# Optimization experiments

Measured on AMD Instinct MI355X. Metric: run time of the kernel, lower is better.

The kernel has to match this reference:

```python
import math
import jax, jax.numpy as jnp
import numpy as np

HIDDEN = 2880
HEAD_DIM = 64
N_HEADS = 64
N_KV = 8
Q_MULT = N_HEADS // N_KV  # 8
QKV_DIM = HEAD_DIM * (N_HEADS + 2 * N_KV)  # 5120
SLIDING_WINDOW = 128
SM_SCALE = 1.0 / math.sqrt(HEAD_DIM)
ROPE_BASE = 150000.0
ROPE_SCALING = 32.0
INIT_CTX = 4096
NTK_ALPHA = 1.0
NTK_BETA = 32.0
EPS = 1e-5
N_TOKENS = 1536


def rope_tables(n):
    # YaRN-style inv_freq mixing (scaling_factor > 1 branch)
    d = HEAD_DIM
    freq = ROPE_BASE ** (jnp.arange(0, d, 2, dtype=jnp.float32) / d)
    concentration = 0.1 * math.log(ROPE_SCALING) + 1.0
    d_half = d / 2
    low = d_half * math.log(INIT_CTX / (NTK_BETA * 2 * math.pi)) / math.log(ROPE_BASE)
    high = d_half * math.log(INIT_CTX / (NTK_ALPHA * 2 * math.pi)) / math.log(ROPE_BASE)
    interpolation = 1.0 / (ROPE_SCALING * freq)
    extrapolation = 1.0 / freq
    ramp = (jnp.arange(d_half, dtype=jnp.float32) - low) / (high - low)
    mask = 1.0 - jnp.clip(ramp, 0.0, 1.0)
    inv_freq = interpolation * (1.0 - mask) + extrapolation * mask
    t = jnp.arange(n, dtype=jnp.float32)
    freqs = t[:, None] * inv_freq[None, :]  # (n, d/2)
    return jnp.cos(freqs) * concentration, jnp.sin(freqs) * concentration


def apply_rotary(x, cos, sin):
    # x: (n, H, d); cos/sin: (n, d/2)
    c = cos[:, None, :]
    s = sin[:, None, :]
    x1, x2 = jnp.split(x, 2, axis=-1)
    return jnp.concatenate([x1 * c - x2 * s, x2 * c + x1 * s], axis=-1)


def setup_inputs() -> dict:
    key = jax.random.key(0)
    ks = jax.random.split(key, 7)
    x = jax.random.normal(ks[0], (N_TOKENS, HIDDEN), dtype=jnp.float32)
    norm_scale = jnp.ones((HIDDEN,), dtype=jnp.float32)
    qkv_w = jax.random.normal(ks[1], (QKV_DIM, HIDDEN), dtype=jnp.float32) * 0.02
    qkv_b = jax.random.normal(ks[2], (QKV_DIM,), dtype=jnp.float32) * 0.02
    out_w = jax.random.normal(ks[3], (HIDDEN, HEAD_DIM * N_HEADS), dtype=jnp.float32) * 0.02
    out_b = jax.random.normal(ks[4], (HIDDEN,), dtype=jnp.float32) * 0.02
    sinks = jax.random.normal(ks[5], (N_HEADS,), dtype=jnp.float32)
    return {"x": x, "norm_scale": norm_scale, "qkv_w": qkv_w, "qkv_b": qkv_b,
            "out_w": out_w, "out_b": out_b, "sinks": sinks}


def reference(x, norm_scale, qkv_w, qkv_b, out_w, out_b, sinks):
    n = x.shape[0]
    # RMSNorm (fp32)
    t = x * jax.lax.rsqrt(jnp.mean(x * x, axis=-1, keepdims=True) + EPS) * norm_scale
    # fused QKV projection
    qkv = t @ qkv_w.T + qkv_b  # (n, QKV_DIM)
    q = qkv[:, : N_HEADS * HEAD_DIM].reshape(n, N_KV, Q_MULT, HEAD_DIM)
    k = qkv[:, N_HEADS * HEAD_DIM : (N_HEADS + N_KV) * HEAD_DIM].reshape(n, N_KV, HEAD_DIM)
    v = qkv[:, (N_HEADS + N_KV) * HEAD_DIM :].reshape(n, N_KV, HEAD_DIM)
    # RoPE
    cos, sin = rope_tables(n)
    q = apply_rotary(q.reshape(n, N_HEADS, HEAD_DIM), cos, sin).reshape(n, N_KV, Q_MULT, HEAD_DIM)
    k = apply_rotary(k, cos, sin)
    # attention with causal + sliding-window mask and sink logits
    i = jnp.arange(n)[:, None]
    j = jnp.arange(n)[None, :]
    allowed = (j <= i) & (j > i - SLIDING_WINDOW)
    mask = jnp.where(allowed, 0.0, -jnp.inf).astype(jnp.float32)  # (q, k)
    scores = jnp.einsum('qhmd,khd->hmqk', q, k) * SM_SCALE + mask[None, None, :, :]
    s = sinks.reshape(N_KV, Q_MULT, 1, 1)
    s = jnp.broadcast_to(s, (N_KV, Q_MULT, n, 1))
    logits = jnp.concatenate([scores, s], axis=-1)
    w = jax.nn.softmax(logits, axis=-1)[..., :-1]  # drop sink column
    attn = jnp.einsum('hmqk,khd->qhmd', w, v).reshape(n, N_HEADS * HEAD_DIM)
    # output projection + residual
    return x + attn @ out_w.T + out_b
```

## Files before the change

### kernel.cpp

```cpp
#include <hip/hip_runtime.h>

typedef __attribute__((ext_vector_type(8))) short bf16x8;
typedef __attribute__((ext_vector_type(4))) float f32x4;

#define HIDDEN 2880
#define QKV_DIM 5120
#define NH 64
#define NKV 8
#define HD 64
#define ATT_DIM 4096
#define WINDOW 128
#define SM_SCALE 0.125f

__device__ __forceinline__ ushort f2bf(float f) {
  union { float f; unsigned u; } a; a.f = f;
  unsigned r = a.u + 0x7fffu + ((a.u >> 16) & 1u);
  return (ushort)(r >> 16);
}
__device__ __forceinline__ float bf2f(ushort u) {
  union { unsigned u; float f; } a; a.u = ((unsigned)u) << 16;
  return a.f;
}

__device__ __forceinline__ void gload_lds16(const void* g, void* l) {
  __builtin_amdgcn_global_load_lds((const __attribute__((address_space(1))) void*)g,
                                   (__attribute__((address_space(3))) void*)l, 16, 0, 0);
}

__global__ __launch_bounds__(256)
void norm_cvt(const float* __restrict__ x, const float* __restrict__ scale,
              ushort* __restrict__ t, int n,
              const float* __restrict__ w, ushort* __restrict__ wout, int n4w) {
  int tid = threadIdx.x;
  if ((int)blockIdx.x >= n) {
    int i = ((int)blockIdx.x - n) * 256 + tid;
    int stride = (gridDim.x - n) * 256;
    for (; i < n4w; i += stride) {
      float4 v = ((const float4*)w)[i];
      ushort4 o = { f2bf(v.x), f2bf(v.y), f2bf(v.z), f2bf(v.w) };
      ((ushort4*)wout)[i] = o;
    }
    return;
  }
  int row = blockIdx.x;
  const float4* xr = (const float4*)(x + (size_t)row * HIDDEN);
  float4 a0 = xr[tid];
  float4 a1 = xr[tid + 256];
  bool has2 = tid < 208;
  float4 a2 = has2 ? xr[tid + 512] : float4{0.f, 0.f, 0.f, 0.f};
  float ss = a0.x*a0.x + a0.y*a0.y + a0.z*a0.z + a0.w*a0.w
           + a1.x*a1.x + a1.y*a1.y + a1.z*a1.z + a1.w*a1.w
           + a2.x*a2.x + a2.y*a2.y + a2.z*a2.z + a2.w*a2.w;
  for (int m = 1; m < 64; m <<= 1) ss += __shfl_xor(ss, m, 64);
  __shared__ float red[4];
  if ((tid & 63) == 0) red[tid >> 6] = ss;
  __syncthreads();
  ss = red[0] + red[1] + red[2] + red[3];
  float r = rsqrtf(ss / (float)HIDDEN + 1e-5f);
  ushort4* tr = (ushort4*)(t + (size_t)row * HIDDEN);
  const float4* sc4 = (const float4*)scale;
  {
    float4 s = sc4[tid];
    ushort4 o = { f2bf(a0.x*r*s.x), f2bf(a0.y*r*s.y), f2bf(a0.z*r*s.z), f2bf(a0.w*r*s.w) };
    tr[tid] = o;
  }
  {
    float4 s = sc4[tid + 256];
    ushort4 o = { f2bf(a1.x*r*s.x), f2bf(a1.y*r*s.y), f2bf(a1.z*r*s.z), f2bf(a1.w*r*s.w) };
    tr[tid + 256] = o;
  }
  if (has2) {
    float4 s = sc4[tid + 512];
    ushort4 o = { f2bf(a2.x*r*s.x), f2bf(a2.y*r*s.y), f2bf(a2.z*r*s.z), f2bf(a2.w*r*s.w) };
    tr[tid + 512] = o;
  }
}

template <int MASK_N>
__global__ __launch_bounds__(512)
void gemm_8p(const ushort* __restrict__ A, const ushort* __restrict__ B,
             ushort* __restrict__ P, int M, int N, int K, int NSK) {
  __shared__ __align__(16) ushort Al[2][256 * 64];
  __shared__ __align__(16) ushort Bl[2][256 * 64];
  const int tid = threadIdx.x;
  const int wave = tid >> 6, lane = tid & 63;
  const int l15 = lane & 15, hi = lane >> 4;

  int nwg = gridDim.x, orig = blockIdx.x;
  int q8 = nwg >> 3, r8 = nwg & 7, xcd = orig & 7, seq = orig >> 3;
  int swz = (xcd < r8 ? xcd * (q8 + 1) : r8 * (q8 + 1) + (xcd - r8) * q8) + seq;
  int nm = M >> 8;
  int bm = swz % nm, bn = swz / nm;
  const int row0 = bm * 256, col0 = bn * 256;
  const int sk = blockIdx.y;
  const int NTtot = K >> 6;
  const int tt0 = sk * NTtot / NSK, tt1 = (sk + 1) * NTtot / NSK;
  ushort* Pp = P + (size_t)sk * M * N;

  const int wrow = (wave >> 2) * 128;
  const int wcol = (wave & 3) * 64;
  const int srow = lane >> 3;
  const int schunk = (lane & 7) ^ srow;

  f32x4 acc[8][4] = {};

  auto stageA = [&](int t, int r) {
    int row = row0 + r * 64 + wave * 8 + srow;
    gload_lds16(A + (size_t)row * K + (t << 6) + schunk * 8,
                &Al[t & 1][(r * 64 + wave * 8) * 64]);
  };
  auto stageB = [&](int t, int r) {
    int brow = col0 + r * 64 + wave * 8 + srow;
    if (MASK_N) { if (brow > N - 1) brow = N - 1; }
    gload_lds16(B + (size_t)brow * K + (t << 6) + schunk * 8,
                &Bl[t & 1][(r * 64 + wave * 8) * 64]);
  };
  auto stageAll = [&](int t) {
#pragma unroll
    for (int r = 0; r < 4; ++r) { stageA(t, r); stageB(t, r); }
  };
  auto LDA = [&](bf16x8 (&dst)[4][2], int mh, const char* base) {
#pragma unroll
    for (int mt = 0; mt < 4; ++mt)
#pragma unroll
      for (int ks = 0; ks < 2; ++ks) {
        int rr = wrow + mh * 64 + mt * 16 + l15;
        int off = (rr * 128 + ks * 64 + hi * 16) ^ ((rr & 7) << 4);
        dst[mt][ks] = *(const bf16x8*)(base + off);
      }
  };
  auto LDB = [&](bf16x8 (&dst)[2][2], int nh, const char* base) {
#pragma unroll
    for (int nt = 0; nt < 2; ++nt)
#pragma unroll
      for (int ks = 0; ks < 2; ++ks) {
        int rr = wcol + nh * 32 + nt * 16 + l15;
        int off = (rr * 128 + ks * 64 + hi * 16) ^ ((rr & 7) << 4);
        dst[nt][ks] = *(const bf16x8*)(base + off);
      }
  };
  auto MMA = [&](bf16x8 (&a)[4][2], bf16x8 (&b)[2][2], int mh, int nh) {
    __builtin_amdgcn_s_setprio(1);
#pragma unroll
    for (int ks = 0; ks < 2; ++ks)
#pragma unroll
      for (int nt = 0; nt < 2; ++nt)
#pragma unroll
        for (int mt = 0; mt < 4; ++mt)
          acc[mh * 4 + mt][nh * 2 + nt] = __builtin_amdgcn_mfma_f32_16x16x32_bf16(
              a[mt][ks], b[nt][ks], acc[mh * 4 + mt][nh * 2 + nt], 0, 0, 0);
    __builtin_amdgcn_s_setprio(0);
  };

  stageAll(tt0);
  bool two = (tt1 - tt0 > 1);
  if (two) {
    stageAll(tt0 + 1);
    asm volatile("s_waitcnt vmcnt(8)" ::: "memory");
  } else {
    asm volatile("s_waitcnt vmcnt(0)" ::: "memory");
  }
  __builtin_amdgcn_s_barrier();

  for (int t = tt0; t < tt1; ++t) {
    const char* Ab = (const char*)&Al[t & 1][0];
    const char* Bb = (const char*)&Bl[t & 1][0];
    bool pre = (t + 2 < tt1);
    bf16x8 afr[4][2], bf0[2][2], bf1[2][2];
    LDA(afr, 0, Ab);
    LDB(bf0, 0, Bb);
    __builtin_amdgcn_s_barrier();
    MMA(afr, bf0, 0, 0);
    __builtin_amdgcn_s_barrier();
    LDB(bf1, 1, Bb);
    if (pre) { stageA(t + 2, 0); stageA(t + 2, 2); }
    __builtin_amdgcn_s_barrier();
    MMA(afr, bf1, 0, 1);
    __builtin_amdgcn_s_barrier();
    LDA(afr, 1, Ab);
    if (pre) { stageB(t + 2, 0); stageB(t + 2, 1); stageB(t + 2, 2); stageB(t + 2, 3); }
    __builtin_amdgcn_s_barrier();
    MMA(afr, bf1, 1, 1);
    __builtin_amdgcn_s_barrier();
    if (pre) { stageA(t + 2, 1); stageA(t + 2, 3); }
    __builtin_amdgcn_s_barrier();
    MMA(afr, bf0, 1, 0);
    if (pre) asm volatile("s_waitcnt vmcnt(8)" ::: "memory");
    else     asm volatile("s_waitcnt vmcnt(0)" ::: "memory");
    __builtin_amdgcn_s_barrier();
  }

#pragma unroll
  for (int mtg = 0; mtg < 8; ++mtg) {
#pragma unroll
    for (int nt = 0; nt < 4; ++nt) {
#pragma unroll
      for (int rr = 0; rr < 4; ++rr) {
        int row = row0 + wrow + mtg * 16 + (hi << 2) + rr;
        int col = col0 + wcol + nt * 16 + l15;
        if (!MASK_N || col < N) Pp[(size_t)row * N + col] = f2bf(acc[mtg][nt][rr]);
      }
    }
  }
}

__global__ __launch_bounds__(256)
void reduce_out(const float* __restrict__ x, const float* __restrict__ b,
                const ushort* __restrict__ p, int nsk, size_t stride,
                float* __restrict__ out, int n4, int N) {
  int i = blockIdx.x * blockDim.x + threadIdx.x;
  if (i >= n4) return;
  float4 v = ((const float4*)x)[i];
  int col = (i * 4) % N;
  float4 bb = *(const float4*)(b + col);
  v.x += bb.x; v.y += bb.y; v.z += bb.z; v.w += bb.w;
  for (int s = 0; s < nsk; ++s) {
    ushort4 pv = *(const ushort4*)(p + s * stride + (size_t)i * 4);
    v.x += bf2f(pv.x); v.y += bf2f(pv.y); v.z += bf2f(pv.z); v.w += bf2f(pv.w);
  }
  ((float4*)out)[i] = v;
}

__global__ __launch_bounds__(256)
void rope_split(const ushort* __restrict__ p, size_t stride, const float* __restrict__ qkvb,
                ushort* __restrict__ qb, ushort* __restrict__ kb, ushort* __restrict__ vb) {
  int tok = blockIdx.x;
  int tid = threadIdx.x;
  __shared__ float cs[32], sn[32];
  if (tid < 32) {
    float d = (float)tid;
    float freq = powf(150000.0f, d / 32.0f);
    float conc = 0.1f * logf(32.0f) + 1.0f;
    float lg = logf(150000.0f);
    float low = 32.0f * logf(4096.0f / (32.0f * 6.2831853f)) / lg;
    float high = 32.0f * logf(4096.0f / 6.2831853f) / lg;
    float ramp = (d - low) / (high - low);
    float cl = fminf(fmaxf(ramp, 0.0f), 1.0f);
    float mask = 1.0f - cl;
    float inv_freq = (1.0f - mask) / (32.0f * freq) + mask / freq;
    float fr = (float)tok * inv_freq;
    cs[tid] = cosf(fr) * conc;
    sn[tid] = sinf(fr) * conc;
  }
  __syncthreads();
  const ushort* r0 = p + (size_t)tok * QKV_DIM;
  const ushort* r1 = r0 + stride;
  auto ld = [&](int c) { return bf2f(r0[c]) + bf2f(r1[c]) + qkvb[c]; };
#pragma unroll
  for (int it = 0; it < 8; ++it) {
    int pp = tid + it * 256;
    int hd = pp >> 5, d = pp & 31;
    float x1 = ld(hd * 64 + d), x2 = ld(hd * 64 + d + 32);
    float c = cs[d], s = sn[d];
    size_t o = ((size_t)tok * NH + hd) * HD + d;
    qb[o] = f2bf(x1 * c - x2 * s);
    qb[o + 32] = f2bf(x2 * c + x1 * s);
  }
  {
    int pp = tid;
    int hd = pp >> 5, d = pp & 31;
    float x1 = ld(4096 + hd * 64 + d), x2 = ld(4096 + hd * 64 + d + 32);
    float c = cs[d], s = sn[d];
    size_t o = ((size_t)tok * NKV + hd) * HD + d;
    kb[o] = f2bf(x1 * c - x2 * s);
    kb[o + 32] = f2bf(x2 * c + x1 * s);
  }
#pragma unroll
  for (int it = 0; it < 2; ++it) {
    int pp = tid + it * 256;
    vb[(size_t)tok * (NKV * HD) + pp] = f2bf(ld(4608 + pp));
  }
}

__global__ __launch_bounds__(512)
void attn_cvt(const ushort* __restrict__ qb, const ushort* __restrict__ kb,
              const ushort* __restrict__ vb, const float* __restrict__ sinks,
              ushort* __restrict__ attn, int n, int nattn,
              const float* __restrict__ w, ushort* __restrict__ wout, int n4w) {
  __shared__ __align__(16) ushort Kl[160 * 64];
  __shared__ __align__(16) ushort Vt[64 * 168];
  __shared__ __align__(16) ushort Pl[8][16 * 40];
  int tid = threadIdx.x;
  if ((int)blockIdx.x >= nattn) {
    int i = ((int)blockIdx.x - nattn) * 512 + tid;
    int stride = (gridDim.x - nattn) * 512;
    for (; i < n4w; i += stride) {
      float4 v = ((const float4*)w)[i];
      ushort4 o = { f2bf(v.x), f2bf(v.y), f2bf(v.z), f2bf(v.w) };
      ((ushort4*)wout)[i] = o;
    }
    return;
  }
  int wave = tid >> 6, lane = tid & 63;
  int l15 = lane & 15, hi = lane >> 4;
  int qstart = ((int)blockIdx.x >> 3) * 16;
  int kv = (int)blockIdx.x & 7;
  int head = kv * 8 + wave;
  int key0 = qstart - 128;

  for (int i = 0; i < 3; ++i) {
    int rowb = i * 64 + wave * 8;
    if (rowb < 160) {
      int r = rowb + (lane >> 3);
      int gj = key0 + r; if (gj < 0) gj = 0;
      int chunk = (lane & 7) ^ (lane >> 3);
      gload_lds16(kb + ((size_t)gj * NKV + kv) * HD + chunk * 8, Kl + rowb * 64);
    }
  }
  for (int e = tid; e < 160 * 16; e += 512) {
    int j = e >> 4, d4 = (e & 15) << 2;
    int gj = key0 + j; if (gj < 0) gj = 0;
    ushort4 v = *(const ushort4*)(vb + ((size_t)gj * NKV + kv) * HD + d4);
    Vt[(d4 + 0) * 168 + j] = v.x;
    Vt[(d4 + 1) * 168 + j] = v.y;
    Vt[(d4 + 2) * 168 + j] = v.z;
    Vt[(d4 + 3) * 168 + j] = v.w;
  }
  bf16x8 qf[2];
#pragma unroll
  for (int ks = 0; ks < 2; ++ks) {
    int r = qstart + l15;
    int kk = ks * 32 + hi * 8;
    qf[ks] = *(const bf16x8*)(qb + ((size_t)r * NH + head) * HD + kk);
  }
  __syncthreads();

  f32x4 s[10] = {};
#pragma unroll
  for (int nt = 0; nt < 10; ++nt) {
#pragma unroll
    for (int ks = 0; ks < 2; ++ks) {
      int r = nt * 16 + l15;
      int off = (r * 128 + (ks * 32 + hi * 8) * 2) ^ ((r & 7) << 4);
      bf16x8 kf = *(const bf16x8*)((const char*)Kl + off);
      s[nt] = __builtin_amdgcn_mfma_f32_16x16x32_bf16(qf[ks], kf, s[nt], 0, 0, 0);
    }
  }

  float lrow[4];
  float snk = sinks[head];
#pragma unroll
  for (int r = 0; r < 4; ++r) {
    int i = qstart + hi * 4 + r;
    float mx = -1e30f;
#pragma unroll
    for (int nt = 0; nt < 10; ++nt) {
      int j = key0 + nt * 16 + l15;
      bool ok = (j >= 0) && (j <= i) && (j > i - WINDOW);
      float val = ok ? s[nt][r] * SM_SCALE : -1e30f;
      s[nt][r] = val;
      mx = fmaxf(mx, val);
    }
    mx = fmaxf(mx, __shfl_xor(mx, 1, 64));
    mx = fmaxf(mx, __shfl_xor(mx, 2, 64));
    mx = fmaxf(mx, __shfl_xor(mx, 4, 64));
    mx = fmaxf(mx, __shfl_xor(mx, 8, 64));
    mx = fmaxf(mx, snk);
    float sum = 0.f;
#pragma unroll
    for (int nt = 0; nt < 10; ++nt) {
      float pv = __expf(s[nt][r] - mx);
      s[nt][r] = pv;
      sum += pv;
    }
    sum += __shfl_xor(sum, 1, 64);
    sum += __shfl_xor(sum, 2, 64);
    sum += __shfl_xor(sum, 4, 64);
    sum += __shfl_xor(sum, 8, 64);
    sum += __expf(snk - mx);
    lrow[r] = sum;
  }

  f32x4 o[4] = {};
#pragma unroll
  for (int kc = 0; kc < 5; ++kc) {
#pragma unroll
    for (int t2 = 0; t2 < 2; ++t2) {
      int nt = kc * 2 + t2;
#pragma unroll
      for (int r = 0; r < 4; ++r)
        Pl[wave][(hi * 4 + r) * 40 + t2 * 16 + l15] = f2bf(s[nt][r]);
    }
    bf16x8 pa = *(const bf16x8*)(&Pl[wave][l15 * 40 + hi * 8]);
#pragma unroll
    for (int nt = 0; nt < 4; ++nt) {
      int d = nt * 16 + l15;
      int kk = kc * 32 + hi * 8;
      bf16x8 vf = *(const bf16x8*)(&Vt[d * 168 + kk]);
      o[nt] = __builtin_amdgcn_mfma_f32_16x16x32_bf16(pa, vf, o[nt], 0, 0, 0);
    }
  }

#pragma unroll
  for (int nt = 0; nt < 4; ++nt)
#pragma unroll
    for (int r = 0; r < 4; ++r) {
      int row = qstart + hi * 4 + r;
      int d = nt * 16 + l15;
      float val = o[nt][r] / lrow[r];
      attn[((size_t)row * NH + head) * HD + d] = f2bf(val);
    }
}

extern "C" void kernel_launch(void* const* d_in, const int* in_sizes, int n_in,
                              void* d_out, int out_size, void* d_ws, size_t ws_size,
                              hipStream_t stream) {
  const float* x      = (const float*)d_in[0];
  const float* nscale = (const float*)d_in[1];
  const float* qkv_w  = (const float*)d_in[2];
  const float* qkv_b  = (const float*)d_in[3];
  const float* out_w  = (const float*)d_in[4];
  const float* out_b  = (const float*)d_in[5];
  const float* sinks  = (const float*)d_in[6];
  float* out = (float*)d_out;
  int n = in_sizes[0] / HIDDEN;

  char* ws = (char*)d_ws;
  size_t off = 0;
  auto alloc = [&](size_t bytes) {
    char* p = ws + off;
    off += (bytes + 255) & ~(size_t)255;
    return p;
  };
  ushort* t_bf    = (ushort*)alloc((size_t)n * HIDDEN * 2);
  ushort* qkvw_bf = (ushort*)alloc((size_t)QKV_DIM * HIDDEN * 2);
  ushort* outw_bf = (ushort*)alloc((size_t)HIDDEN * ATT_DIM * 2);
  ushort* q_bf    = (ushort*)alloc((size_t)n * NH * HD * 2);
  ushort* k_bf    = (ushort*)alloc((size_t)n * NKV * HD * 2);
  ushort* v_bf    = (ushort*)alloc((size_t)n * NKV * HD * 2);
  ushort* attn    = (ushort*)alloc((size_t)n * ATT_DIM * 2);
  size_t qkv_ps = (size_t)n * QKV_DIM;
  size_t out_ps = (size_t)n * HIDDEN;
  size_t pelems = 2 * qkv_ps > 3 * out_ps ? 2 * qkv_ps : 3 * out_ps;
  ushort* partials = (ushort*)alloc(pelems * 2);

  norm_cvt<<<n + 1024, 256, 0, stream>>>(x, nscale, t_bf, n,
                                         qkv_w, qkvw_bf, QKV_DIM * HIDDEN / 4);
  gemm_8p<0><<<dim3((n / 256) * (QKV_DIM / 256), 2), 512, 0, stream>>>(
      t_bf, qkvw_bf, partials, n, QKV_DIM, HIDDEN, 2);
  rope_split<<<n, 256, 0, stream>>>(partials, qkv_ps, qkv_b, q_bf, k_bf, v_bf);
  int nattn = (n / 16) * NKV;
  attn_cvt<<<nattn + 320, 512, 0, stream>>>(q_bf, k_bf, v_bf, sinks, attn, n, nattn,
                                            out_w, outw_bf, HIDDEN * ATT_DIM / 4);
  gemm_8p<1><<<dim3((n / 256) * 12, 3), 512, 0, stream>>>(
      attn, outw_bf, partials, n, HIDDEN, ATT_DIM, 3);
  reduce_out<<<(n * HIDDEN / 4 + 255) / 256, 256, 0, stream>>>(
      x, out_b, partials, 3, out_ps, out, n * HIDDEN / 4, HIDDEN);
}
```

Baseline: 171.1 us.

## Fuse split-K reduction, bias and RoPE into the attention kernel

```diff
diff --git a/kernel.cpp b/kernel.cpp
--- a/kernel.cpp
+++ b/kernel.cpp
@@ -221,107 +221,119 @@
   ((float4*)out)[i] = v;
 }
 
-__global__ __launch_bounds__(256)
-void rope_split(const ushort* __restrict__ p, size_t stride, const float* __restrict__ qkvb,
-                ushort* __restrict__ qb, ushort* __restrict__ kb, ushort* __restrict__ vb) {
-  int tok = blockIdx.x;
+__global__ __launch_bounds__(512)
+void attn_cvt(const ushort* __restrict__ p, size_t stride, const float* __restrict__ qkvb,
+              const float* __restrict__ sinks, ushort* __restrict__ attn, int n, int nattn,
+              const float* __restrict__ w, ushort* __restrict__ wout, int n4w) {
+  __shared__ __align__(16) ushort Kl[160 * 64];
+  __shared__ __align__(16) ushort Vt[64 * 168];
+  __shared__ __align__(16) ushort Pl[8][16 * 40];
+  __shared__ float invf[32];
+  __shared__ float conc_s;
   int tid = threadIdx.x;
-  __shared__ float cs[32], sn[32];
+  if ((int)blockIdx.x >= nattn) {
+    int i = ((int)blockIdx.x - nattn) * 512 + tid;
+    int gstride = (gridDim.x - nattn) * 512;
+    for (; i < n4w; i += gstride) {
+      float4 v = ((const float4*)w)[i];
+      ushort4 o = { f2bf(v.x), f2bf(v.y), f2bf(v.z), f2bf(v.w) };
+      ((ushort4*)wout)[i] = o;
+    }
+    return;
+  }
+  int wave = tid >> 6, lane = tid & 63;
+  int l15 = lane & 15, hi = lane >> 4;
+  int qstart = ((int)blockIdx.x >> 3) * 16;
+  int kv = (int)blockIdx.x & 7;
+  int head = kv * 8 + wave;
+  int key0 = qstart - 128;
+
   if (tid < 32) {
     float d = (float)tid;
     float freq = powf(150000.0f, d / 32.0f);
-    float conc = 0.1f * logf(32.0f) + 1.0f;
     float lg = logf(150000.0f);
     float low = 32.0f * logf(4096.0f / (32.0f * 6.2831853f)) / lg;
     float high = 32.0f * logf(4096.0f / 6.2831853f) / lg;
     float ramp = (d - low) / (high - low);
     float cl = fminf(fmaxf(ramp, 0.0f), 1.0f);
     float mask = 1.0f - cl;
-    float inv_freq = (1.0f - mask) / (32.0f * freq) + mask / freq;
-    float fr = (float)tok * inv_freq;
-    cs[tid] = cosf(fr) * conc;
-    sn[tid] = sinf(fr) * conc;
+    invf[tid] = (1.0f - mask) / (32.0f * freq) + mask / freq;
+    if (tid == 0) conc_s = 0.1f * logf(32.0f) + 1.0f;
   }
   __syncthreads();
-  const ushort* r0 = p + (size_t)tok * QKV_DIM;
-  const ushort* r1 = r0 + stride;
-  auto ld = [&](int c) { return bf2f(r0[c]) + bf2f(r1[c]) + qkvb[c]; };
-#pragma unroll
-  for (int it = 0; it < 8; ++it) {
-    int pp = tid + it * 256;
-    int hd = pp >> 5, d = pp & 31;
-    float x1 = ld(hd * 64 + d), x2 = ld(hd * 64 + d + 32);
-    float c = cs[d], s = sn[d];
-    size_t o = ((size_t)tok * NH + hd) * HD + d;
-    qb[o] = f2bf(x1 * c - x2 * s);
-    qb[o + 32] = f2bf(x2 * c + x1 * s);
-  }
-  {
-    int pp = tid;
-    int hd = pp >> 5, d = pp & 31;
-    float x1 = ld(4096 + hd * 64 + d), x2 = ld(4096 + hd * 64 + d + 32);
-    float c = cs[d], s = sn[d];
-    size_t o = ((size_t)tok * NKV + hd) * HD + d;
-    kb[o] = f2bf(x1 * c - x2 * s);
-    kb[o + 32] = f2bf(x2 * c + x1 * s);
-  }
-#pragma unroll
-  for (int it = 0; it < 2; ++it) {
-    int pp = tid + it * 256;
-    vb[(size_t)tok * (NKV * HD) + pp] = f2bf(ld(4608 + pp));
-  }
-}
-
-__global__ __launch_bounds__(512)
-void attn_cvt(const ushort* __restrict__ qb, const ushort* __restrict__ kb,
-              const ushort* __restrict__ vb, const float* __restrict__ sinks,
-              ushort* __restrict__ attn, int n, int nattn,
-              const float* __restrict__ w, ushort* __restrict__ wout, int n4w) {
-  __shared__ __align__(16) ushort Kl[160 * 64];
-  __shared__ __align__(16) ushort Vt[64 * 168];
-  __shared__ __align__(16) ushort Pl[8][16 * 40];
-  int tid = threadIdx.x;
-  if ((int)blockIdx.x >= nattn) {
-    int i = ((int)blockIdx.x - nattn) * 512 + tid;
-    int stride = (gridDim.x - nattn) * 512;
-    for (; i < n4w; i += stride) {
-      float4 v = ((const float4*)w)[i];
-      ushort4 o = { f2bf(v.x), f2bf(v.y), f2bf(v.z), f2bf(v.w) };
-      ((ushort4*)wout)[i] = o;
-    }
-    return;
-  }
-  int wave = tid >> 6, lane = tid & 63;
-  int l15 = lane & 15, hi = lane >> 4;
-  int qstart = ((int)blockIdx.x >> 3) * 16;
-  int kv = (int)blockIdx.x & 7;
-  int head = kv * 8 + wave;
-  int key0 = qstart - 128;
+  float conc = conc_s;
+
+  const ushort* r0b = p;
+  const ushort* r1b = p + stride;
 
   for (int i = 0; i < 3; ++i) {
-    int rowb = i * 64 + wave * 8;
-    if (rowb < 160) {
-      int r = rowb + (lane >> 3);
-      int gj = key0 + r; if (gj < 0) gj = 0;
-      int chunk = (lane & 7) ^ (lane >> 3);
-      gload_lds16(kb + ((size_t)gj * NKV + kv) * HD + chunk * 8, Kl + rowb * 64);
+    int task = tid + i * 512;
+    if (task < 1280) {
+      int rb = task >> 3, ch = task & 7;
+      int gj = key0 + rb; if (gj < 0) gj = 0;
+      size_t base = (size_t)gj * QKV_DIM + 4096 + kv * 64;
+      int d0 = ch * 8, d0p = d0 ^ 32;
+      bf16x8 a0 = *(const bf16x8*)(r0b + base + d0);
+      bf16x8 a1 = *(const bf16x8*)(r1b + base + d0);
+      bf16x8 b0 = *(const bf16x8*)(r0b + base + d0p);
+      bf16x8 b1 = *(const bf16x8*)(r1b + base + d0p);
+      bf16x8 o;
+#pragma unroll
+      for (int j = 0; j < 8; ++j) {
+        float xv = bf2f((ushort)a0[j]) + bf2f((ushort)a1[j]) + qkvb[4096 + kv * 64 + d0 + j];
+        float yv = bf2f((ushort)b0[j]) + bf2f((ushort)b1[j]) + qkvb[4096 + kv * 64 + d0p + j];
+        int d31 = (d0 + j) & 31;
+        float fr = (float)gj * invf[d31];
+        float c, s;
+        __sincosf(fr, &s, &c);
+        c *= conc; s *= conc;
+        float v = (d0 < 32) ? (xv * c - yv * s) : (xv * c + yv * s);
+        o[j] = (short)f2bf(v);
+      }
+      int off = (rb * 128 + ch * 16) ^ ((rb & 7) << 4);
+      *(bf16x8*)((char*)Kl + off) = o;
     }
   }
   for (int e = tid; e < 160 * 16; e += 512) {
     int j = e >> 4, d4 = (e & 15) << 2;
     int gj = key0 + j; if (gj < 0) gj = 0;
-    ushort4 v = *(const ushort4*)(vb + ((size_t)gj * NKV + kv) * HD + d4);
-    Vt[(d4 + 0) * 168 + j] = v.x;
-    Vt[(d4 + 1) * 168 + j] = v.y;
-    Vt[(d4 + 2) * 168 + j] = v.z;
-    Vt[(d4 + 3) * 168 + j] = v.w;
+    size_t base = (size_t)gj * QKV_DIM + 4608 + kv * 64 + d4;
+    ushort4 v0 = *(const ushort4*)(r0b + base);
+    ushort4 v1 = *(const ushort4*)(r1b + base);
+    const float* bb = qkvb + 4608 + kv * 64 + d4;
+    Vt[(d4 + 0) * 168 + j] = f2bf(bf2f(v0.x) + bf2f(v1.x) + bb[0]);
+    Vt[(d4 + 1) * 168 + j] = f2bf(bf2f(v0.y) + bf2f(v1.y) + bb[1]);
+    Vt[(d4 + 2) * 168 + j] = f2bf(bf2f(v0.z) + bf2f(v1.z) + bb[2]);
+    Vt[(d4 + 3) * 168 + j] = f2bf(bf2f(v0.w) + bf2f(v1.w) + bb[3]);
   }
   bf16x8 qf[2];
-#pragma unroll
-  for (int ks = 0; ks < 2; ++ks) {
-    int r = qstart + l15;
-    int kk = ks * 32 + hi * 8;
-    qf[ks] = *(const bf16x8*)(qb + ((size_t)r * NH + head) * HD + kk);
+  {
+    int tok = qstart + l15;
+    size_t base = (size_t)tok * QKV_DIM + head * 64;
+    float cs8[8], sn8[8];
+#pragma unroll
+    for (int j = 0; j < 8; ++j) {
+      int d31 = hi * 8 + j;
+      float fr = (float)tok * invf[d31];
+      float c, s;
+      __sincosf(fr, &s, &c);
+      cs8[j] = c * conc; sn8[j] = s * conc;
+    }
+#pragma unroll
+    for (int ks = 0; ks < 2; ++ks) {
+      int d0 = ks * 32 + hi * 8, d0p = d0 ^ 32;
+      bf16x8 a0 = *(const bf16x8*)(r0b + base + d0);
+      bf16x8 a1 = *(const bf16x8*)(r1b + base + d0);
+      bf16x8 b0 = *(const bf16x8*)(r0b + base + d0p);
+      bf16x8 b1 = *(const bf16x8*)(r1b + base + d0p);
+#pragma unroll
+      for (int j = 0; j < 8; ++j) {
+        float xv = bf2f((ushort)a0[j]) + bf2f((ushort)a1[j]) + qkvb[head * 64 + d0 + j];
+        float yv = bf2f((ushort)b0[j]) + bf2f((ushort)b1[j]) + qkvb[head * 64 + d0p + j];
+        float v = (ks == 0) ? (xv * cs8[j] - yv * sn8[j]) : (xv * cs8[j] + yv * sn8[j]);
+        qf[ks][j] = (short)f2bf(v);
+      }
+    }
   }
   __syncthreads();
 
@@ -425,9 +437,6 @@
   ushort* t_bf    = (ushort*)alloc((size_t)n * HIDDEN * 2);
   ushort* qkvw_bf = (ushort*)alloc((size_t)QKV_DIM * HIDDEN * 2);
   ushort* outw_bf = (ushort*)alloc((size_t)HIDDEN * ATT_DIM * 2);
-  ushort* q_bf    = (ushort*)alloc((size_t)n * NH * HD * 2);
-  ushort* k_bf    = (ushort*)alloc((size_t)n * NKV * HD * 2);
-  ushort* v_bf    = (ushort*)alloc((size_t)n * NKV * HD * 2);
   ushort* attn    = (ushort*)alloc((size_t)n * ATT_DIM * 2);
   size_t qkv_ps = (size_t)n * QKV_DIM;
   size_t out_ps = (size_t)n * HIDDEN;
@@ -438,9 +447,8 @@
                                          qkv_w, qkvw_bf, QKV_DIM * HIDDEN / 4);
   gemm_8p<0><<<dim3((n / 256) * (QKV_DIM / 256), 2), 512, 0, stream>>>(
       t_bf, qkvw_bf, partials, n, QKV_DIM, HIDDEN, 2);
-  rope_split<<<n, 256, 0, stream>>>(partials, qkv_ps, qkv_b, q_bf, k_bf, v_bf);
   int nattn = (n / 16) * NKV;
-  attn_cvt<<<nattn + 320, 512, 0, stream>>>(q_bf, k_bf, v_bf, sinks, attn, n, nattn,
+  attn_cvt<<<nattn + 320, 512, 0, stream>>>(partials, qkv_ps, qkv_b, sinks, attn, n, nattn,
                                             out_w, outw_bf, HIDDEN * ATT_DIM / 4);
   gemm_8p<1><<<dim3((n / 256) * 12, 3), 512, 0, stream>>>(
       attn, outw_bf, partials, n, HIDDEN, ATT_DIM, 3);
```

After: 157.5 us, median of 2. -7.9%, faster.
